# Performance work log

Hardware: AMD Instinct MI355X
Metric: run time of the kernel (lower is better)

The kernel has to match this reference:

```python
import jax, jax.numpy as jnp
import numpy as np

LATENT_DIM = 512
ASSET_DIM = 8192


def setup_inputs() -> dict:
    key = jax.random.key(0)
    ks = jax.random.split(key, 7)
    d = LATENT_DIM
    s = 1.0 / np.sqrt(d)  # torch Linear default init scale (uniform bound)
    z = jax.random.normal(ks[0], (ASSET_DIM, d), dtype=jnp.float32)
    Wq = jax.random.uniform(ks[1], (d, d), jnp.float32, -s, s)
    Wk = jax.random.uniform(ks[2], (d, d), jnp.float32, -s, s)
    Wv = jax.random.uniform(ks[3], (d, d), jnp.float32, -s, s)
    bq = jax.random.uniform(ks[4], (d,), jnp.float32, -s, s)
    bk = jax.random.uniform(ks[5], (d,), jnp.float32, -s, s)
    bv = jax.random.uniform(ks[6], (d,), jnp.float32, -s, s)
    return {"z": z, "Wq": Wq, "bq": bq, "Wk": Wk, "bk": bk, "Wv": Wv, "bv": bv}


def reference(z, Wq, bq, Wk, bk, Wv, bv):
    # z: (N, D). Single-head self-attention over assets.
    d = z.shape[-1]
    scale = d ** (-0.5)
    q = z @ Wq.T + bq          # (N, D)
    k = z @ Wk.T + bk          # (N, D)
    v = z @ Wv.T + bv          # (N, D)
    scores = jnp.einsum('nd,md->nm', q, k) * scale   # (N, N)
    attn = jax.nn.softmax(scores, axis=-1)
    # Original does attn[:, :, None] * v[None] then sum(dim=1); identical math:
    h = attn @ v               # (N, D)
    return h
```

## Files before the change

### kernel.cpp

```cpp
#include <hip/hip_runtime.h>
#include <hip/hip_bf16.h>
#include <stdint.h>

#define D 512
#define N 8192

typedef __attribute__((ext_vector_type(8))) short short8;
typedef __attribute__((ext_vector_type(4))) float f32x4;

static __device__ __forceinline__ unsigned short f2bf(float f) {
  unsigned int u = __builtin_bit_cast(unsigned int, f);
  u += 0x7fffu + ((u >> 16) & 1u);
  return (unsigned short)(u >> 16);
}
static __device__ __forceinline__ float bf2f(unsigned short s) {
  unsigned int u = ((unsigned int)s) << 16;
  return __builtin_bit_cast(float, u);
}

typedef const __attribute__((address_space(1))) unsigned int* gas_ptr;
typedef __attribute__((address_space(3))) unsigned int* las_ptr;
static __device__ __forceinline__ void gload_lds16(const void* g, void* l) {
  __builtin_amdgcn_global_load_lds((gas_ptr)g, (las_ptr)l, 16, 0, 0);
}

__global__ void cast_z_k(const float* __restrict__ z, unsigned short* __restrict__ zb) {
  int i = blockIdx.x * 256 + threadIdx.x;
  const int n4 = N * D / 4;
  for (; i < n4; i += gridDim.x * 256) {
    float4 v = ((const float4*)z)[i];
    ushort4 o = { f2bf(v.x), f2bf(v.y), f2bf(v.z), f2bf(v.w) };
    ((ushort4*)zb)[i] = o;
  }
}

__global__ void cast_w_k(const float* __restrict__ Wq, const float* __restrict__ Wk,
                         const float* __restrict__ Wv, const float* __restrict__ bq,
                         const float* __restrict__ bk, const float* __restrict__ bv,
                         unsigned short* __restrict__ wb, float* __restrict__ bqkv) {
  const float scale = 0.044194173824159216f;
  int i = blockIdx.x * 256 + threadIdx.x;
  const int per = D * D / 4;
  if (i < 3 * per) {
    int sec = i / per;
    int w4 = i - sec * per;
    const float* W = sec == 0 ? Wq : (sec == 1 ? Wk : Wv);
    float s = sec == 0 ? scale : 1.0f;
    float4 v = ((const float4*)W)[w4];
    ushort4 o = { f2bf(v.x * s), f2bf(v.y * s), f2bf(v.z * s), f2bf(v.w * s) };
    ((ushort4*)wb)[sec * per + w4] = o;
  }
  if (i < 3 * D) {
    int sec = i >> 9, j = i & (D - 1);
    const float* b = sec == 0 ? bq : (sec == 1 ? bk : bv);
    bqkv[i] = b[j] * (sec == 0 ? scale : 1.0f);
  }
}

#define BM 128
#define BN 128
#define BK 64

template <int EPI>
__global__ __launch_bounds__(256) void gemm_nt(
    const unsigned short* __restrict__ A, int lda,
    const unsigned short* __restrict__ B, int ldb,
    int K, int tiles_n,
    const float* __restrict__ bias,
    unsigned short* __restrict__ o0, unsigned short* __restrict__ o1,
    unsigned short* __restrict__ o2,
    float* __restrict__ lpart) {
  __shared__ unsigned short Ash[2][BM * BK];
  __shared__ unsigned short Bsh[2][BN * BK];

  const int t = threadIdx.x;
  const int w = t >> 6, lane = t & 63;
  const int bid = blockIdx.x, nwg = gridDim.x;
  const int cpx = nwg >> 3;
  const int swz = (bid & 7) * cpx + (bid >> 3);
  int tm, tn, kt0 = 0, nkt = K / BK, sidx = 0;
  if constexpr (EPI == 3) {
    sidx = swz >> 8;
    const int tile = swz & 255;
    tm = tile >> 2;
    tn = tile & 3;
    kt0 = sidx * 43;
    nkt = (sidx < 2) ? 43 : 42;
  } else {
    tm = swz / tiles_n;
    tn = swz - tm * tiles_n;
  }
  const int row0 = tm * BM, col0 = tn * BN;

  const int srow = t >> 3;
  const int scol = ((t & 7) ^ ((t >> 3) & 7)) * 8;
  const unsigned short* Ab = A + (size_t)(row0 + srow) * lda + scol;
  const unsigned short* Bb = B + (size_t)(col0 + srow) * ldb + scol;
  const int ldsbase = (w * 64) * 8;

  const int l15 = lane & 15, lhi = lane >> 4, lx = lane & 7;
  const int wr = w >> 1, wc = w & 1;
  const int arow = (wr * 64 + l15) * BK;
  const int brow = (wc * 64 + l15) * BK;
  const int ko0 = ((0 + lhi) ^ lx) * 8;
  const int ko1 = ((4 + lhi) ^ lx) * 8;

  f32x4 acc[4][4] = {};

  auto stage = [&](int buf, int k0) {
    const unsigned short* a = Ab + k0;
    const unsigned short* b = Bb + k0;
    unsigned short* la = &Ash[buf][ldsbase];
    unsigned short* lb = &Bsh[buf][ldsbase];
#pragma unroll
    for (int i = 0; i < 4; ++i) {
      gload_lds16(a + (size_t)(i * 32) * lda, la + i * 2048);
      gload_lds16(b + (size_t)(i * 32) * ldb, lb + i * 2048);
    }
  };

  stage(0, kt0 * BK);
  asm volatile("s_waitcnt vmcnt(0)" ::: "memory");
  __syncthreads();
  int cur = 0;
  for (int kt = 0; kt < nkt; ++kt) {
    if (kt + 1 < nkt) stage(cur ^ 1, (kt0 + kt + 1) * BK);
    const unsigned short* As = Ash[cur];
    const unsigned short* Bs = Bsh[cur];
#pragma unroll
    for (int ks = 0; ks < 2; ++ks) {
      const int ko = ks ? ko1 : ko0;
      short8 af[4], bg[4];
#pragma unroll
      for (int rf = 0; rf < 4; ++rf)
        af[rf] = *(const short8*)(As + arow + rf * (16 * BK) + ko);
#pragma unroll
      for (int cf = 0; cf < 4; ++cf)
        bg[cf] = *(const short8*)(Bs + brow + cf * (16 * BK) + ko);
#pragma unroll
      for (int rf = 0; rf < 4; ++rf)
#pragma unroll
        for (int cf = 0; cf < 4; ++cf)
          acc[rf][cf] = __builtin_amdgcn_mfma_f32_16x16x32_bf16(af[rf], bg[cf], acc[rf][cf], 0, 0, 0);
    }
    asm volatile("s_waitcnt vmcnt(0)" ::: "memory");
    __syncthreads();
    cur ^= 1;
  }

  const int r0g = row0 + wr * 64;
  const int c0g = col0 + wc * 64;

  if constexpr (EPI == 0) {
    const int sec = col0 >> 9;
#pragma unroll
    for (int cf = 0; cf < 4; ++cf) {
      const int c = c0g + cf * 16 + l15;
      const int cj = c & (D - 1);
      const float bb = bias[c];
#pragma unroll
      for (int rf = 0; rf < 4; ++rf) {
        const int r = r0g + rf * 16 + lhi * 4;
        f32x4 v = acc[rf][cf];
        if (sec == 0) {
#pragma unroll
          for (int g = 0; g < 4; ++g) o0[(size_t)(r + g) * D + cj] = f2bf(v[g] + bb);
        } else if (sec == 1) {
#pragma unroll
          for (int g = 0; g < 4; ++g) o1[(size_t)(r + g) * D + cj] = f2bf(v[g] + bb);
        } else {
          ushort4 o = { f2bf(v[0] + bb), f2bf(v[1] + bb), f2bf(v[2] + bb), f2bf(v[3] + bb) };
          *(ushort4*)(o2 + (size_t)cj * N + r) = o;
        }
      }
    }
  }

  if constexpr (EPI == 1) {
    float rs[4][4];
#pragma unroll
    for (int rf = 0; rf < 4; ++rf)
#pragma unroll
      for (int g = 0; g < 4; ++g) rs[rf][g] = 0.f;
#pragma unroll
    for (int cf = 0; cf < 4; ++cf) {
      const int c = c0g + cf * 16 + l15;
#pragma unroll
      for (int rf = 0; rf < 4; ++rf) {
        const int r = r0g + rf * 16 + lhi * 4;
        f32x4 v = acc[rf][cf];
#pragma unroll
        for (int g = 0; g < 4; ++g) {
          unsigned short us = f2bf(__expf(v[g]));
          o0[(size_t)(r + g) * N + c] = us;
          rs[rf][g] += bf2f(us);
        }
      }
    }
#pragma unroll
    for (int rf = 0; rf < 4; ++rf)
#pragma unroll
      for (int g = 0; g < 4; ++g) {
        float s = rs[rf][g];
        s += __shfl_xor(s, 1);
        s += __shfl_xor(s, 2);
        s += __shfl_xor(s, 4);
        s += __shfl_xor(s, 8);
        rs[rf][g] = s;
      }
    if (l15 == 0) {
      const int slot = tn * 2 + wc;
#pragma unroll
      for (int rf = 0; rf < 4; ++rf)
#pragma unroll
        for (int g = 0; g < 4; ++g)
          lpart[(size_t)slot * N + r0g + rf * 16 + lhi * 4 + g] = rs[rf][g];
    }
  }

  if constexpr (EPI == 3) {
    unsigned short* op = o0 + (size_t)sidx * ((size_t)N * D);
#pragma unroll
    for (int cf = 0; cf < 4; ++cf) {
      const int c = c0g + cf * 16 + l15;
#pragma unroll
      for (int rf = 0; rf < 4; ++rf) {
        const int r = r0g + rf * 16 + lhi * 4;
        f32x4 v = acc[rf][cf];
#pragma unroll
        for (int g = 0; g < 4; ++g) op[(size_t)(r + g) * D + c] = f2bf(v[g]);
      }
    }
  }
}

__global__ void linv_k(const float* __restrict__ lpart, float* __restrict__ linv) {
  const int m = blockIdx.x * 256 + threadIdx.x;
  float s = 0.f;
  for (int i = 0; i < 128; ++i) s += lpart[(size_t)i * N + m];
  linv[m] = 1.0f / s;
}

__global__ void reduce_k(const unsigned short* __restrict__ Opart,
                         const float* __restrict__ linv, float* __restrict__ out) {
  const int i = blockIdx.x * 256 + threadIdx.x;
  const int m = i >> 7;
  const float li = linv[m];
  const size_t nd = (size_t)N * D;
  ushort4 a = ((const ushort4*)Opart)[i];
  ushort4 b = ((const ushort4*)(Opart + nd))[i];
  ushort4 c = ((const ushort4*)(Opart + 2 * nd))[i];
  float4 o;
  o.x = (bf2f(a.x) + bf2f(b.x) + bf2f(c.x)) * li;
  o.y = (bf2f(a.y) + bf2f(b.y) + bf2f(c.y)) * li;
  o.z = (bf2f(a.z) + bf2f(b.z) + bf2f(c.z)) * li;
  o.w = (bf2f(a.w) + bf2f(b.w) + bf2f(c.w)) * li;
  ((float4*)out)[i] = o;
}

extern "C" void kernel_launch(void* const* d_in, const int* in_sizes, int n_in,
                              void* d_out, int out_size, void* d_ws, size_t ws_size,
                              hipStream_t stream) {
  const float* z  = (const float*)d_in[0];
  const float* Wq = (const float*)d_in[1];
  const float* bq = (const float*)d_in[2];
  const float* Wk = (const float*)d_in[3];
  const float* bk = (const float*)d_in[4];
  const float* Wv = (const float*)d_in[5];
  const float* bv = (const float*)d_in[6];
  float* out = (float*)d_out;

  char* ws = (char*)d_ws;
  unsigned short* zb = (unsigned short*)(ws + 0);
  unsigned short* qb = (unsigned short*)(ws + 8388608);
  unsigned short* kb = (unsigned short*)(ws + 16777216);
  unsigned short* vT = (unsigned short*)(ws + 25165824);
  unsigned short* wb = (unsigned short*)(ws + 33554432);
  float* linv       = (float*)(ws + 33554432);
  float* bqkv       = (float*)(ws + 35127296);
  float* lpart      = (float*)(ws + 35133440);
  unsigned short* P = (unsigned short*)(ws + 39327744);
  unsigned short* Opart = (unsigned short*)(ws + 0);

  cast_z_k<<<dim3(2048), dim3(256), 0, stream>>>(z, zb);
  cast_w_k<<<dim3(768), dim3(256), 0, stream>>>(Wq, Wk, Wv, bq, bk, bv, wb, bqkv);

  gemm_nt<0><<<dim3(64 * 12), dim3(256), 0, stream>>>(
      zb, D, wb, D, D, 12, bqkv, qb, kb, vT, (float*)nullptr);

  gemm_nt<1><<<dim3(64 * 64), dim3(256), 0, stream>>>(
      qb, D, kb, D, D, 64, (const float*)nullptr, P, (unsigned short*)nullptr,
      (unsigned short*)nullptr, lpart);

  linv_k<<<dim3(32), dim3(256), 0, stream>>>(lpart, linv);

  gemm_nt<3><<<dim3(768), dim3(256), 0, stream>>>(
      P, N, vT, N, N, 4, (const float*)nullptr, Opart, (unsigned short*)nullptr,
      (unsigned short*)nullptr, (float*)nullptr);

  reduce_k<<<dim3(4096), dim3(256), 0, stream>>>(Opart, linv, out);
}
```

Before: 269.4 us.

## Replace QK^T exp GEMM with 256x256-tile 8-phase pipelined kernel

Adds a dedicated QK^T kernel that computes exp(scores), writes P and the per-row partial sums. It uses 256x256 output tiles, 512 threads and a double-buffered LDS schedule split into eight phases, with fine-grained barriers and raised MFMA priority. It replaces the generic 128x128 gemm_nt<1> path. The aim is more operand reuse per tile and overlap of global-to-LDS loads with MFMA work. In exchange it uses a large LDS footprint (about 128KB), which limits occupancy, and a more fragile hand-scheduled synchronisation pattern.

```diff
diff --git a/kernel.cpp b/kernel.cpp
--- a/kernel.cpp
+++ b/kernel.cpp
@@ -68,8 +68,7 @@
     int K, int tiles_n,
     const float* __restrict__ bias,
     unsigned short* __restrict__ o0, unsigned short* __restrict__ o1,
-    unsigned short* __restrict__ o2,
-    float* __restrict__ lpart) {
+    unsigned short* __restrict__ o2) {
   __shared__ unsigned short Ash[2][BM * BK];
   __shared__ unsigned short Bsh[2][BN * BK];
 
@@ -176,12 +175,8 @@
     }
   }
 
-  if constexpr (EPI == 1) {
-    float rs[4][4];
-#pragma unroll
-    for (int rf = 0; rf < 4; ++rf)
-#pragma unroll
-      for (int g = 0; g < 4; ++g) rs[rf][g] = 0.f;
+  if constexpr (EPI == 3) {
+    unsigned short* op = o0 + (size_t)sidx * ((size_t)N * D);
 #pragma unroll
     for (int cf = 0; cf < 4; ++cf) {
       const int c = c0g + cf * 16 + l15;
@@ -190,48 +185,168 @@
         const int r = r0g + rf * 16 + lhi * 4;
         f32x4 v = acc[rf][cf];
 #pragma unroll
-        for (int g = 0; g < 4; ++g) {
-          unsigned short us = f2bf(__expf(v[g]));
-          o0[(size_t)(r + g) * N + c] = us;
-          rs[rf][g] += bf2f(us);
-        }
-      }
-    }
-#pragma unroll
-    for (int rf = 0; rf < 4; ++rf)
-#pragma unroll
-      for (int g = 0; g < 4; ++g) {
-        float s = rs[rf][g];
-        s += __shfl_xor(s, 1);
-        s += __shfl_xor(s, 2);
-        s += __shfl_xor(s, 4);
-        s += __shfl_xor(s, 8);
-        rs[rf][g] = s;
-      }
-    if (l15 == 0) {
-      const int slot = tn * 2 + wc;
-#pragma unroll
-      for (int rf = 0; rf < 4; ++rf)
-#pragma unroll
-        for (int g = 0; g < 4; ++g)
-          lpart[(size_t)slot * N + r0g + rf * 16 + lhi * 4 + g] = rs[rf][g];
-    }
-  }
-
-  if constexpr (EPI == 3) {
-    unsigned short* op = o0 + (size_t)sidx * ((size_t)N * D);
-#pragma unroll
-    for (int cf = 0; cf < 4; ++cf) {
-      const int c = c0g + cf * 16 + l15;
-#pragma unroll
-      for (int rf = 0; rf < 4; ++rf) {
-        const int r = r0g + rf * 16 + lhi * 4;
-        f32x4 v = acc[rf][cf];
-#pragma unroll
         for (int g = 0; g < 4; ++g) op[(size_t)(r + g) * D + c] = f2bf(v[g]);
       }
     }
   }
+}
+
+__global__ __launch_bounds__(512, 2) void qk_exp_8ph(
+    const unsigned short* __restrict__ A,
+    const unsigned short* __restrict__ B,
+    unsigned short* __restrict__ P,
+    float* __restrict__ lpart) {
+  __shared__ unsigned short Ash[2][256 * 64];
+  __shared__ unsigned short Bsh[2][256 * 64];
+
+  const int t = threadIdx.x;
+  const int w = t >> 6, lane = t & 63;
+  const int bid = blockIdx.x;
+  const int swz = (bid & 7) * 128 + (bid >> 3);
+  const int tm = swz >> 5, tn = swz & 31;
+  const int row0 = tm * 256, col0 = tn * 256;
+
+  const int wr = w >> 2, wc = w & 3;
+  const int l15 = lane & 15, lhi = lane >> 4, lx = lane & 7;
+
+  const int sr = t >> 3;
+  const int ss = ((t & 7) ^ (sr & 7)) * 8;
+  const unsigned short* Ab = A + (size_t)(row0 + sr) * D + ss;
+  const unsigned short* Bb = B + (size_t)(col0 + sr) * D + ss;
+  const int ldst = t * 8;
+
+  const int aRowB = (wr * 128 + l15) * 64;
+  const int bRowB = (wc * 64 + l15) * 64;
+  const int sl0 = ((0 + lhi) ^ lx) * 8;
+  const int sl1 = ((4 + lhi) ^ lx) * 8;
+
+  f32x4 acc[8][4] = {};
+  short8 af[4][2], bf[2][2];
+
+#define STAGE8(buf, kt)                                                     \
+  do {                                                                      \
+    const unsigned short* a_ = Ab + (kt) * 64;                              \
+    const unsigned short* b_ = Bb + (kt) * 64;                              \
+    unsigned short* la_ = &Ash[buf][0];                                     \
+    unsigned short* lb_ = &Bsh[buf][0];                                     \
+    gload_lds16(a_, la_ + ldst);                                            \
+    gload_lds16(a_ + (size_t)64 * D, la_ + 4096 + ldst);                    \
+    gload_lds16(a_ + (size_t)128 * D, la_ + 8192 + ldst);                   \
+    gload_lds16(a_ + (size_t)192 * D, la_ + 12288 + ldst);                  \
+    gload_lds16(b_, lb_ + ldst);                                            \
+    gload_lds16(b_ + (size_t)64 * D, lb_ + 4096 + ldst);                    \
+    gload_lds16(b_ + (size_t)128 * D, lb_ + 8192 + ldst);                   \
+    gload_lds16(b_ + (size_t)192 * D, lb_ + 12288 + ldst);                  \
+  } while (0)
+
+#define RDA(kk, mh)                                                          \
+  do {                                                                       \
+    _Pragma("unroll") for (int fm = 0; fm < 4; ++fm) {                       \
+      const unsigned short* p_ = &Ash[kk][aRowB + (mh) * 4096 + fm * 1024];  \
+      af[fm][0] = *(const short8*)(p_ + sl0);                                \
+      af[fm][1] = *(const short8*)(p_ + sl1);                                \
+    }                                                                        \
+  } while (0)
+
+#define RDB(kk, nh)                                                          \
+  do {                                                                       \
+    _Pragma("unroll") for (int fn = 0; fn < 2; ++fn) {                       \
+      const unsigned short* p_ = &Bsh[kk][bRowB + (nh) * 2048 + fn * 1024];  \
+      bf[fn][0] = *(const short8*)(p_ + sl0);                                \
+      bf[fn][1] = *(const short8*)(p_ + sl1);                                \
+    }                                                                        \
+  } while (0)
+
+#define MMA(mh, nh)                                                          \
+  do {                                                                       \
+    __builtin_amdgcn_s_setprio(1);                                           \
+    _Pragma("unroll") for (int ks = 0; ks < 2; ++ks)                         \
+      _Pragma("unroll") for (int fm = 0; fm < 4; ++fm)                       \
+        _Pragma("unroll") for (int fn = 0; fn < 2; ++fn)                     \
+          acc[(mh) * 4 + fm][(nh) * 2 + fn] =                                \
+              __builtin_amdgcn_mfma_f32_16x16x32_bf16(                       \
+                  af[fm][ks], bf[fn][ks], acc[(mh) * 4 + fm][(nh) * 2 + fn], \
+                  0, 0, 0);                                                  \
+    __builtin_amdgcn_s_setprio(0);                                           \
+  } while (0)
+
+#define BARLG()                                         \
+  do {                                                  \
+    __builtin_amdgcn_s_barrier();                       \
+    asm volatile("s_waitcnt lgkmcnt(0)" ::: "memory");  \
+    __builtin_amdgcn_sched_barrier(0);                  \
+  } while (0)
+
+#define VMDRAIN() asm volatile("s_waitcnt vmcnt(0)" ::: "memory")
+#define POSTBAR() __builtin_amdgcn_s_barrier()
+
+  STAGE8(0, 0);
+  VMDRAIN();
+  __builtin_amdgcn_s_barrier();
+
+  const int NI = (D / 64) / 2;
+  for (int i = 0; i < NI; ++i) {
+    RDA(0, 0); RDB(0, 0);
+    STAGE8(1, 2 * i + 1);
+    BARLG(); MMA(0, 0); POSTBAR();
+
+    RDB(0, 1);
+    BARLG(); MMA(0, 1); POSTBAR();
+
+    RDA(0, 1);
+    BARLG(); MMA(1, 1); POSTBAR();
+
+    RDB(0, 0);
+    VMDRAIN();
+    BARLG(); MMA(1, 0); POSTBAR();
+
+    RDA(1, 0); RDB(1, 0);
+    if (i + 1 < NI) STAGE8(0, 2 * i + 2);
+    BARLG(); MMA(0, 0); POSTBAR();
+
+    RDB(1, 1);
+    BARLG(); MMA(0, 1); POSTBAR();
+
+    RDA(1, 1);
+    BARLG(); MMA(1, 1); POSTBAR();
+
+    RDB(1, 0);
+    if (i + 1 < NI) VMDRAIN();
+    BARLG(); MMA(1, 0); POSTBAR();
+  }
+
+#pragma unroll
+  for (int fm = 0; fm < 8; ++fm) {
+    const int r = row0 + wr * 128 + fm * 16 + lhi * 4;
+    float rs[4] = {0.f, 0.f, 0.f, 0.f};
+#pragma unroll
+    for (int fn = 0; fn < 4; ++fn) {
+      const int c = col0 + wc * 64 + fn * 16 + l15;
+      f32x4 v = acc[fm][fn];
+#pragma unroll
+      for (int g = 0; g < 4; ++g) {
+        unsigned short us = f2bf(__expf(v[g]));
+        P[(size_t)(r + g) * N + c] = us;
+        rs[g] += bf2f(us);
+      }
+    }
+#pragma unroll
+    for (int g = 0; g < 4; ++g) {
+      float s = rs[g];
+      s += __shfl_xor(s, 1);
+      s += __shfl_xor(s, 2);
+      s += __shfl_xor(s, 4);
+      s += __shfl_xor(s, 8);
+      if (l15 == 0) lpart[(size_t)(tn * 4 + wc) * N + r + g] = s;
+    }
+  }
+#undef STAGE8
+#undef RDA
+#undef RDB
+#undef MMA
+#undef BARLG
+#undef VMDRAIN
+#undef POSTBAR
 }
 
 __global__ void linv_k(const float* __restrict__ lpart, float* __restrict__ linv) {
@@ -286,17 +401,15 @@
   cast_w_k<<<dim3(768), dim3(256), 0, stream>>>(Wq, Wk, Wv, bq, bk, bv, wb, bqkv);
 
   gemm_nt<0><<<dim3(64 * 12), dim3(256), 0, stream>>>(
-      zb, D, wb, D, D, 12, bqkv, qb, kb, vT, (float*)nullptr);
-
-  gemm_nt<1><<<dim3(64 * 64), dim3(256), 0, stream>>>(
-      qb, D, kb, D, D, 64, (const float*)nullptr, P, (unsigned short*)nullptr,
-      (unsigned short*)nullptr, lpart);
+      zb, D, wb, D, D, 12, bqkv, qb, kb, vT);
+
+  qk_exp_8ph<<<dim3(1024), dim3(512), 0, stream>>>(qb, kb, P, lpart);
 
   linv_k<<<dim3(32), dim3(256), 0, stream>>>(lpart, linv);
 
   gemm_nt<3><<<dim3(768), dim3(256), 0, stream>>>(
       P, N, vT, N, N, 4, (const float*)nullptr, Opart, (unsigned short*)nullptr,
-      (unsigned short*)nullptr, (float*)nullptr);
+      (unsigned short*)nullptr);
 
   reduce_k<<<dim3(4096), dim3(256), 0, stream>>>(Opart, linv, out);
 }
```

Result: faster. 254.1 us (-5.7%).

## Rewrite GEMMs as 512-thread kernels with 4-deep LDS ring pipeline

Applied to the files above, without the earlier changes.

Replaces the 256-thread double-buffered GEMM with a 512-thread (8-wave) kernel that keeps a 4-slot LDS ring with two stages in flight, partial waitcnts, raw s_barrier and setprio around the MFMA block. It also reduces row sums per block in LDS (halving lpart slots), uses nontemporal stores for P and partial outputs, and moves the PV split-K from 3 to 4 splits, with the fourth written directly to fp32 out and folded in by reduce_k. The aim is to overlap global loads with MFMA and cut partial-sum traffic, at the cost of more LDS per block (128KB), which may limit occupancy.

```diff
diff --git a/kernel.cpp b/kernel.cpp
--- a/kernel.cpp
+++ b/kernel.cpp
@@ -57,111 +57,113 @@
   }
 }
 
-#define BM 128
-#define BN 128
-#define BK 64
-
 template <int EPI>
-__global__ __launch_bounds__(256) void gemm_nt(
+__global__ __launch_bounds__(512) void mm128_ring(
     const unsigned short* __restrict__ A, int lda,
     const unsigned short* __restrict__ B, int ldb,
-    int K, int tiles_n,
     const float* __restrict__ bias,
     unsigned short* __restrict__ o0, unsigned short* __restrict__ o1,
     unsigned short* __restrict__ o2,
-    float* __restrict__ lpart) {
-  __shared__ unsigned short Ash[2][BM * BK];
-  __shared__ unsigned short Bsh[2][BN * BK];
+    float* __restrict__ lpart, float* __restrict__ outF) {
+  __shared__ unsigned short Ash[4][128 * 64];
+  __shared__ unsigned short Bsh[4][128 * 64];
 
   const int t = threadIdx.x;
   const int w = t >> 6, lane = t & 63;
-  const int bid = blockIdx.x, nwg = gridDim.x;
-  const int cpx = nwg >> 3;
-  const int swz = (bid & 7) * cpx + (bid >> 3);
-  int tm, tn, kt0 = 0, nkt = K / BK, sidx = 0;
-  if constexpr (EPI == 3) {
-    sidx = swz >> 8;
-    const int tile = swz & 255;
-    tm = tile >> 2;
-    tn = tile & 3;
-    kt0 = sidx * 43;
-    nkt = (sidx < 2) ? 43 : 42;
+  const int wr = w >> 2, wc = w & 3;
+  const int l15 = lane & 15, lhi = lane >> 4, lx = lane & 7;
+  const int bid = blockIdx.x;
+
+  int tm, tn, kt0 = 0, nkt, sp = 0;
+  if constexpr (EPI == 0) {
+    const int swz = (bid & 7) * 96 + (bid >> 3);
+    tm = swz / 12; tn = swz - tm * 12; nkt = 8;
+  } else if constexpr (EPI == 1) {
+    const int swz = (bid & 7) * 512 + (bid >> 3);
+    tm = swz >> 6; tn = swz & 63; nkt = 8;
   } else {
-    tm = swz / tiles_n;
-    tn = swz - tm * tiles_n;
-  }
-  const int row0 = tm * BM, col0 = tn * BN;
-
-  const int srow = t >> 3;
-  const int scol = ((t & 7) ^ ((t >> 3) & 7)) * 8;
-  const unsigned short* Ab = A + (size_t)(row0 + srow) * lda + scol;
-  const unsigned short* Bb = B + (size_t)(col0 + srow) * ldb + scol;
-  const int ldsbase = (w * 64) * 8;
-
-  const int l15 = lane & 15, lhi = lane >> 4, lx = lane & 7;
-  const int wr = w >> 1, wc = w & 1;
-  const int arow = (wr * 64 + l15) * BK;
-  const int brow = (wc * 64 + l15) * BK;
-  const int ko0 = ((0 + lhi) ^ lx) * 8;
-  const int ko1 = ((4 + lhi) ^ lx) * 8;
-
-  f32x4 acc[4][4] = {};
-
-  auto stage = [&](int buf, int k0) {
-    const unsigned short* a = Ab + k0;
-    const unsigned short* b = Bb + k0;
-    unsigned short* la = &Ash[buf][ldsbase];
-    unsigned short* lb = &Bsh[buf][ldsbase];
-#pragma unroll
-    for (int i = 0; i < 4; ++i) {
-      gload_lds16(a + (size_t)(i * 32) * lda, la + i * 2048);
-      gload_lds16(b + (size_t)(i * 32) * ldb, lb + i * 2048);
-    }
+    const int swz = (bid & 7) * 128 + (bid >> 3);
+    sp = swz >> 8;
+    const int idx = swz & 255;
+    tm = idx >> 2; tn = idx & 3;
+    kt0 = sp * 32; nkt = 32;
+  }
+  const int row0 = tm * 128, col0 = tn * 128;
+
+  const int sr = t >> 3;
+  const int sc = ((t & 7) ^ (sr & 7)) * 8;
+  const unsigned short* Ab = A + (size_t)(row0 + sr) * lda + sc;
+  const unsigned short* Bb = B + (size_t)(col0 + sr) * ldb + sc;
+  const int dst = t * 8;
+
+  const int arow = (wr * 64 + l15) * 64;
+  const int brow = (wc * 32 + l15) * 64;
+  const int sl0 = ((0 + lhi) ^ lx) * 8;
+  const int sl1 = ((4 + lhi) ^ lx) * 8;
+
+  f32x4 acc[4][2] = {};
+
+  auto stage = [&](int buf, int kt) {
+    const unsigned short* a = Ab + (size_t)(kt0 + kt) * 64;
+    const unsigned short* b = Bb + (size_t)(kt0 + kt) * 64;
+    gload_lds16(a, &Ash[buf][dst]);
+    gload_lds16(a + (size_t)64 * lda, &Ash[buf][4096 + dst]);
+    gload_lds16(b, &Bsh[buf][dst]);
+    gload_lds16(b + (size_t)64 * ldb, &Bsh[buf][4096 + dst]);
   };
 
-  stage(0, kt0 * BK);
-  asm volatile("s_waitcnt vmcnt(0)" ::: "memory");
-  __syncthreads();
-  int cur = 0;
+  stage(0, 0);
+  stage(1, 1);
+  asm volatile("s_waitcnt vmcnt(4)" ::: "memory");
+  __builtin_amdgcn_s_barrier();
+
   for (int kt = 0; kt < nkt; ++kt) {
-    if (kt + 1 < nkt) stage(cur ^ 1, (kt0 + kt + 1) * BK);
-    const unsigned short* As = Ash[cur];
-    const unsigned short* Bs = Bsh[cur];
-#pragma unroll
-    for (int ks = 0; ks < 2; ++ks) {
-      const int ko = ks ? ko1 : ko0;
-      short8 af[4], bg[4];
-#pragma unroll
-      for (int rf = 0; rf < 4; ++rf)
-        af[rf] = *(const short8*)(As + arow + rf * (16 * BK) + ko);
-#pragma unroll
-      for (int cf = 0; cf < 4; ++cf)
-        bg[cf] = *(const short8*)(Bs + brow + cf * (16 * BK) + ko);
-#pragma unroll
-      for (int rf = 0; rf < 4; ++rf)
-#pragma unroll
-        for (int cf = 0; cf < 4; ++cf)
-          acc[rf][cf] = __builtin_amdgcn_mfma_f32_16x16x32_bf16(af[rf], bg[cf], acc[rf][cf], 0, 0, 0);
-    }
-    asm volatile("s_waitcnt vmcnt(0)" ::: "memory");
-    __syncthreads();
-    cur ^= 1;
-  }
-
-  const int r0g = row0 + wr * 64;
-  const int c0g = col0 + wc * 64;
+    const int kb = kt & 3;
+    short8 af[4][2], bg[2][2];
+#pragma unroll
+    for (int fm = 0; fm < 4; ++fm) {
+      const unsigned short* p = &Ash[kb][arow + fm * 1024];
+      af[fm][0] = *(const short8*)(p + sl0);
+      af[fm][1] = *(const short8*)(p + sl1);
+    }
+#pragma unroll
+    for (int fn = 0; fn < 2; ++fn) {
+      const unsigned short* p = &Bsh[kb][brow + fn * 1024];
+      bg[fn][0] = *(const short8*)(p + sl0);
+      bg[fn][1] = *(const short8*)(p + sl1);
+    }
+    if (kt + 2 < nkt) {
+      stage((kt + 2) & 3, kt + 2);
+      asm volatile("s_waitcnt vmcnt(4)" ::: "memory");
+    } else {
+      asm volatile("s_waitcnt vmcnt(0)" ::: "memory");
+    }
+    __builtin_amdgcn_s_barrier();
+    asm volatile("s_waitcnt lgkmcnt(0)" ::: "memory");
+    __builtin_amdgcn_sched_barrier(0);
+    __builtin_amdgcn_s_setprio(1);
+#pragma unroll
+    for (int ks = 0; ks < 2; ++ks)
+#pragma unroll
+      for (int fm = 0; fm < 4; ++fm)
+#pragma unroll
+        for (int fn = 0; fn < 2; ++fn)
+          acc[fm][fn] = __builtin_amdgcn_mfma_f32_16x16x32_bf16(
+              af[fm][ks], bg[fn][ks], acc[fm][fn], 0, 0, 0);
+    __builtin_amdgcn_s_setprio(0);
+  }
 
   if constexpr (EPI == 0) {
-    const int sec = col0 >> 9;
-#pragma unroll
-    for (int cf = 0; cf < 4; ++cf) {
-      const int c = c0g + cf * 16 + l15;
+    const int sec = tn >> 2;
+#pragma unroll
+    for (int fn = 0; fn < 2; ++fn) {
+      const int c = col0 + wc * 32 + fn * 16 + l15;
       const int cj = c & (D - 1);
       const float bb = bias[c];
 #pragma unroll
-      for (int rf = 0; rf < 4; ++rf) {
-        const int r = r0g + rf * 16 + lhi * 4;
-        f32x4 v = acc[rf][cf];
+      for (int fm = 0; fm < 4; ++fm) {
+        const int r = row0 + wr * 64 + fm * 16 + lhi * 4;
+        f32x4 v = acc[fm][fn];
         if (sec == 0) {
 #pragma unroll
           for (int g = 0; g < 4; ++g) o0[(size_t)(r + g) * D + cj] = f2bf(v[g] + bb);
@@ -179,56 +181,78 @@
   if constexpr (EPI == 1) {
     float rs[4][4];
 #pragma unroll
-    for (int rf = 0; rf < 4; ++rf)
-#pragma unroll
-      for (int g = 0; g < 4; ++g) rs[rf][g] = 0.f;
-#pragma unroll
-    for (int cf = 0; cf < 4; ++cf) {
-      const int c = c0g + cf * 16 + l15;
-#pragma unroll
-      for (int rf = 0; rf < 4; ++rf) {
-        const int r = r0g + rf * 16 + lhi * 4;
-        f32x4 v = acc[rf][cf];
+    for (int fm = 0; fm < 4; ++fm)
+#pragma unroll
+      for (int g = 0; g < 4; ++g) rs[fm][g] = 0.f;
+#pragma unroll
+    for (int fn = 0; fn < 2; ++fn) {
+      const int c = col0 + wc * 32 + fn * 16 + l15;
+#pragma unroll
+      for (int fm = 0; fm < 4; ++fm) {
+        const int r = row0 + wr * 64 + fm * 16 + lhi * 4;
+        f32x4 v = acc[fm][fn];
 #pragma unroll
         for (int g = 0; g < 4; ++g) {
           unsigned short us = f2bf(__expf(v[g]));
-          o0[(size_t)(r + g) * N + c] = us;
-          rs[rf][g] += bf2f(us);
+          __builtin_nontemporal_store(us, &o0[(size_t)(r + g) * N + c]);
+          rs[fm][g] += bf2f(us);
         }
       }
     }
 #pragma unroll
-    for (int rf = 0; rf < 4; ++rf)
+    for (int fm = 0; fm < 4; ++fm)
 #pragma unroll
       for (int g = 0; g < 4; ++g) {
-        float s = rs[rf][g];
+        float s = rs[fm][g];
         s += __shfl_xor(s, 1);
         s += __shfl_xor(s, 2);
         s += __shfl_xor(s, 4);
         s += __shfl_xor(s, 8);
-        rs[rf][g] = s;
-      }
+        rs[fm][g] = s;
+      }
+    __builtin_amdgcn_s_barrier();
+    float* lred = (float*)&Ash[0][0];
     if (l15 == 0) {
-      const int slot = tn * 2 + wc;
-#pragma unroll
-      for (int rf = 0; rf < 4; ++rf)
+#pragma unroll
+      for (int fm = 0; fm < 4; ++fm)
 #pragma unroll
         for (int g = 0; g < 4; ++g)
-          lpart[(size_t)slot * N + r0g + rf * 16 + lhi * 4 + g] = rs[rf][g];
+          lred[wc * 128 + wr * 64 + fm * 16 + lhi * 4 + g] = rs[fm][g];
+    }
+    __syncthreads();
+    if (t < 128) {
+      float s = lred[t] + lred[128 + t] + lred[256 + t] + lred[384 + t];
+      lpart[(size_t)tn * N + row0 + t] = s;
     }
   }
 
   if constexpr (EPI == 3) {
-    unsigned short* op = o0 + (size_t)sidx * ((size_t)N * D);
-#pragma unroll
-    for (int cf = 0; cf < 4; ++cf) {
-      const int c = c0g + cf * 16 + l15;
-#pragma unroll
-      for (int rf = 0; rf < 4; ++rf) {
-        const int r = r0g + rf * 16 + lhi * 4;
-        f32x4 v = acc[rf][cf];
-#pragma unroll
-        for (int g = 0; g < 4; ++g) op[(size_t)(r + g) * D + c] = f2bf(v[g]);
+    if (sp < 3) {
+      unsigned short* op = o0 + (size_t)sp * ((size_t)N * D);
+#pragma unroll
+      for (int fn = 0; fn < 2; ++fn) {
+        const int c = col0 + wc * 32 + fn * 16 + l15;
+#pragma unroll
+        for (int fm = 0; fm < 4; ++fm) {
+          const int r = row0 + wr * 64 + fm * 16 + lhi * 4;
+          f32x4 v = acc[fm][fn];
+#pragma unroll
+          for (int g = 0; g < 4; ++g)
+            __builtin_nontemporal_store(f2bf(v[g]), &op[(size_t)(r + g) * D + c]);
+        }
+      }
+    } else {
+#pragma unroll
+      for (int fn = 0; fn < 2; ++fn) {
+        const int c = col0 + wc * 32 + fn * 16 + l15;
+#pragma unroll
+        for (int fm = 0; fm < 4; ++fm) {
+          const int r = row0 + wr * 64 + fm * 16 + lhi * 4;
+          f32x4 v = acc[fm][fn];
+#pragma unroll
+          for (int g = 0; g < 4; ++g)
+            __builtin_nontemporal_store(v[g], &outF[(size_t)(r + g) * D + c]);
+        }
       }
     }
   }
@@ -237,7 +261,7 @@
 __global__ void linv_k(const float* __restrict__ lpart, float* __restrict__ linv) {
   const int m = blockIdx.x * 256 + threadIdx.x;
   float s = 0.f;
-  for (int i = 0; i < 128; ++i) s += lpart[(size_t)i * N + m];
+  for (int i = 0; i < 64; ++i) s += lpart[(size_t)i * N + m];
   linv[m] = 1.0f / s;
 }
 
@@ -250,11 +274,11 @@
   ushort4 a = ((const ushort4*)Opart)[i];
   ushort4 b = ((const ushort4*)(Opart + nd))[i];
   ushort4 c = ((const ushort4*)(Opart + 2 * nd))[i];
-  float4 o;
-  o.x = (bf2f(a.x) + bf2f(b.x) + bf2f(c.x)) * li;
-  o.y = (bf2f(a.y) + bf2f(b.y) + bf2f(c.y)) * li;
-  o.z = (bf2f(a.z) + bf2f(b.z) + bf2f(c.z)) * li;
-  o.w = (bf2f(a.w) + bf2f(b.w) + bf2f(c.w)) * li;
+  float4 o = ((float4*)out)[i];
+  o.x = (bf2f(a.x) + bf2f(b.x) + bf2f(c.x) + o.x) * li;
+  o.y = (bf2f(a.y) + bf2f(b.y) + bf2f(c.y) + o.y) * li;
+  o.z = (bf2f(a.z) + bf2f(b.z) + bf2f(c.z) + o.z) * li;
+  o.w = (bf2f(a.w) + bf2f(b.w) + bf2f(c.w) + o.w) * li;
   ((float4*)out)[i] = o;
 }
 
@@ -285,18 +309,18 @@
   cast_z_k<<<dim3(2048), dim3(256), 0, stream>>>(z, zb);
   cast_w_k<<<dim3(768), dim3(256), 0, stream>>>(Wq, Wk, Wv, bq, bk, bv, wb, bqkv);
 
-  gemm_nt<0><<<dim3(64 * 12), dim3(256), 0, stream>>>(
-      zb, D, wb, D, D, 12, bqkv, qb, kb, vT, (float*)nullptr);
-
-  gemm_nt<1><<<dim3(64 * 64), dim3(256), 0, stream>>>(
-      qb, D, kb, D, D, 64, (const float*)nullptr, P, (unsigned short*)nullptr,
-      (unsigned short*)nullptr, lpart);
+  mm128_ring<0><<<dim3(768), dim3(512), 0, stream>>>(
+      zb, D, wb, D, bqkv, qb, kb, vT, (float*)nullptr, (float*)nullptr);
+
+  mm128_ring<1><<<dim3(4096), dim3(512), 0, stream>>>(
+      qb, D, kb, D, (const float*)nullptr, P, (unsigned short*)nullptr,
+      (unsigned short*)nullptr, lpart, (float*)nullptr);
 
   linv_k<<<dim3(32), dim3(256), 0, stream>>>(lpart, linv);
 
-  gemm_nt<3><<<dim3(768), dim3(256), 0, stream>>>(
-      P, N, vT, N, N, 4, (const float*)nullptr, Opart, (unsigned short*)nullptr,
-      (unsigned short*)nullptr, (float*)nullptr);
+  mm128_ring<3><<<dim3(1024), dim3(512), 0, stream>>>(
+      P, N, vT, N, (const float*)nullptr, Opart, (unsigned short*)nullptr,
+      (unsigned short*)nullptr, (float*)nullptr, out);
 
   reduce_k<<<dim3(4096), dim3(256), 0, stream>>>(Opart, linv, out);
 }
```

Result: slower. 303.4 us (+12.6%).

## Fuse QK^T, exp and PV into a split-KV attention kernel

Applied to the files above, without the earlier changes.

Replaces the separate scores GEMM (which wrote the full N×N exp matrix to global memory) and the PV GEMM with one fused kernel. Each block handles 128 query rows against a 2048-key split, holding the exp tile in LDS and accumulating P·V in registers. The fourth split writes fp32 straight into the output, and the reduce kernel adds it in. This removes roughly 128MB of P traffic, but uses no running max, only 256 blocks of 512 threads at one block per CU, and no double-buffering of the V loads.

```diff
diff --git a/kernel.cpp b/kernel.cpp
--- a/kernel.cpp
+++ b/kernel.cpp
@@ -57,51 +57,32 @@
   }
 }
 
-#define BM 128
-#define BN 128
-#define BK 64
-
-template <int EPI>
-__global__ __launch_bounds__(256) void gemm_nt(
-    const unsigned short* __restrict__ A, int lda,
-    const unsigned short* __restrict__ B, int ldb,
-    int K, int tiles_n,
+__global__ __launch_bounds__(256) void proj_qkv(
+    const unsigned short* __restrict__ A,
+    const unsigned short* __restrict__ B,
     const float* __restrict__ bias,
     unsigned short* __restrict__ o0, unsigned short* __restrict__ o1,
-    unsigned short* __restrict__ o2,
-    float* __restrict__ lpart) {
-  __shared__ unsigned short Ash[2][BM * BK];
-  __shared__ unsigned short Bsh[2][BN * BK];
+    unsigned short* __restrict__ o2) {
+  __shared__ unsigned short Ash[2][128 * 64];
+  __shared__ unsigned short Bsh[2][128 * 64];
 
   const int t = threadIdx.x;
   const int w = t >> 6, lane = t & 63;
-  const int bid = blockIdx.x, nwg = gridDim.x;
-  const int cpx = nwg >> 3;
-  const int swz = (bid & 7) * cpx + (bid >> 3);
-  int tm, tn, kt0 = 0, nkt = K / BK, sidx = 0;
-  if constexpr (EPI == 3) {
-    sidx = swz >> 8;
-    const int tile = swz & 255;
-    tm = tile >> 2;
-    tn = tile & 3;
-    kt0 = sidx * 43;
-    nkt = (sidx < 2) ? 43 : 42;
-  } else {
-    tm = swz / tiles_n;
-    tn = swz - tm * tiles_n;
-  }
-  const int row0 = tm * BM, col0 = tn * BN;
+  const int bid = blockIdx.x;
+  const int swz = (bid & 7) * 96 + (bid >> 3);
+  const int tm = swz / 12, tn = swz - tm * 12;
+  const int row0 = tm * 128, col0 = tn * 128;
 
   const int srow = t >> 3;
   const int scol = ((t & 7) ^ ((t >> 3) & 7)) * 8;
-  const unsigned short* Ab = A + (size_t)(row0 + srow) * lda + scol;
-  const unsigned short* Bb = B + (size_t)(col0 + srow) * ldb + scol;
+  const unsigned short* Ab = A + (size_t)(row0 + srow) * D + scol;
+  const unsigned short* Bb = B + (size_t)(col0 + srow) * D + scol;
   const int ldsbase = (w * 64) * 8;
 
   const int l15 = lane & 15, lhi = lane >> 4, lx = lane & 7;
   const int wr = w >> 1, wc = w & 1;
-  const int arow = (wr * 64 + l15) * BK;
-  const int brow = (wc * 64 + l15) * BK;
+  const int arow = (wr * 64 + l15) * 64;
+  const int brow = (wc * 64 + l15) * 64;
   const int ko0 = ((0 + lhi) ^ lx) * 8;
   const int ko1 = ((4 + lhi) ^ lx) * 8;
 
@@ -114,17 +95,17 @@
     unsigned short* lb = &Bsh[buf][ldsbase];
 #pragma unroll
     for (int i = 0; i < 4; ++i) {
-      gload_lds16(a + (size_t)(i * 32) * lda, la + i * 2048);
-      gload_lds16(b + (size_t)(i * 32) * ldb, lb + i * 2048);
+      gload_lds16(a + (size_t)(i * 32) * D, la + i * 2048);
+      gload_lds16(b + (size_t)(i * 32) * D, lb + i * 2048);
     }
   };
 
-  stage(0, kt0 * BK);
+  stage(0, 0);
   asm volatile("s_waitcnt vmcnt(0)" ::: "memory");
   __syncthreads();
   int cur = 0;
-  for (int kt = 0; kt < nkt; ++kt) {
-    if (kt + 1 < nkt) stage(cur ^ 1, (kt0 + kt + 1) * BK);
+  for (int kt = 0; kt < 8; ++kt) {
+    if (kt + 1 < 8) stage(cur ^ 1, (kt + 1) * 64);
     const unsigned short* As = Ash[cur];
     const unsigned short* Bs = Bsh[cur];
 #pragma unroll
@@ -133,10 +114,10 @@
       short8 af[4], bg[4];
 #pragma unroll
       for (int rf = 0; rf < 4; ++rf)
-        af[rf] = *(const short8*)(As + arow + rf * (16 * BK) + ko);
+        af[rf] = *(const short8*)(As + arow + rf * (16 * 64) + ko);
 #pragma unroll
       for (int cf = 0; cf < 4; ++cf)
-        bg[cf] = *(const short8*)(Bs + brow + cf * (16 * BK) + ko);
+        bg[cf] = *(const short8*)(Bs + brow + cf * (16 * 64) + ko);
 #pragma unroll
       for (int rf = 0; rf < 4; ++rf)
 #pragma unroll
@@ -150,94 +131,208 @@
 
   const int r0g = row0 + wr * 64;
   const int c0g = col0 + wc * 64;
-
-  if constexpr (EPI == 0) {
-    const int sec = col0 >> 9;
-#pragma unroll
-    for (int cf = 0; cf < 4; ++cf) {
-      const int c = c0g + cf * 16 + l15;
-      const int cj = c & (D - 1);
-      const float bb = bias[c];
-#pragma unroll
-      for (int rf = 0; rf < 4; ++rf) {
-        const int r = r0g + rf * 16 + lhi * 4;
-        f32x4 v = acc[rf][cf];
-        if (sec == 0) {
-#pragma unroll
-          for (int g = 0; g < 4; ++g) o0[(size_t)(r + g) * D + cj] = f2bf(v[g] + bb);
-        } else if (sec == 1) {
-#pragma unroll
-          for (int g = 0; g < 4; ++g) o1[(size_t)(r + g) * D + cj] = f2bf(v[g] + bb);
-        } else {
-          ushort4 o = { f2bf(v[0] + bb), f2bf(v[1] + bb), f2bf(v[2] + bb), f2bf(v[3] + bb) };
-          *(ushort4*)(o2 + (size_t)cj * N + r) = o;
+  const int sec = col0 >> 9;
+#pragma unroll
+  for (int cf = 0; cf < 4; ++cf) {
+    const int c = c0g + cf * 16 + l15;
+    const int cj = c & (D - 1);
+    const float bb = bias[c];
+#pragma unroll
+    for (int rf = 0; rf < 4; ++rf) {
+      const int r = r0g + rf * 16 + lhi * 4;
+      f32x4 v = acc[rf][cf];
+      if (sec == 0) {
+#pragma unroll
+        for (int g = 0; g < 4; ++g) o0[(size_t)(r + g) * D + cj] = f2bf(v[g] + bb);
+      } else if (sec == 1) {
+#pragma unroll
+        for (int g = 0; g < 4; ++g) o1[(size_t)(r + g) * D + cj] = f2bf(v[g] + bb);
+      } else {
+        ushort4 o = { f2bf(v[0] + bb), f2bf(v[1] + bb), f2bf(v[2] + bb), f2bf(v[3] + bb) };
+        *(ushort4*)(o2 + (size_t)cj * N + r) = o;
+      }
+    }
+  }
+}
+
+__global__ __launch_bounds__(512, 1) void fused_attn(
+    const unsigned short* __restrict__ qb,
+    const unsigned short* __restrict__ kb,
+    const unsigned short* __restrict__ vT,
+    unsigned short* __restrict__ Opart,
+    float* __restrict__ outF,
+    float* __restrict__ lpart) {
+  __shared__ unsigned short SA[2][128 * 32];
+  __shared__ unsigned short SB[2][256 * 32];
+  __shared__ unsigned short PL[128 * 260];
+  __shared__ unsigned short VB[512 * 32];
+
+  const int t = threadIdx.x;
+  const int w = t >> 6, lane = t & 63;
+  const int wr = w >> 2, wc = w & 3;
+  const int l15 = lane & 15, lhi = lane >> 4;
+  const int l3 = l15 & 3;
+
+  const int bid = blockIdx.x;
+  const int xcd = bid & 7, loc = bid >> 3;
+  const int sp = xcd >> 1;
+  const int qt = loc + 32 * (xcd & 1);
+  const int r0 = qt * 128;
+  const int kv0 = sp * 2048;
+
+  const int ssl = (t & 3) ^ ((t >> 2) & 3);
+  const unsigned short* qsrc = qb + (size_t)(r0 + (t >> 2)) * D + ssl * 8;
+  const unsigned short* ksrc = kb + (size_t)(kv0 + (t >> 2)) * D + ssl * 8;
+  const unsigned short* vsrc = vT + (size_t)(t >> 2) * N + kv0 + ssl * 8;
+  const int sdst = t * 8;
+
+  const int aoff = (wr * 64 + l15) * 32 + ((lhi ^ l3) << 3);
+  const int boff = (wc * 64 + l15) * 32 + ((lhi ^ l3) << 3);
+  const int voff = (wc * 128 + l15) * 32 + ((lhi ^ l3) << 3);
+  const int poff = (wr * 64 + l15) * 260 + (lhi << 3);
+
+  f32x4 acc_o[4][8] = {};
+  float rs_acc[4][4] = {{0.f,0.f,0.f,0.f},{0.f,0.f,0.f,0.f},{0.f,0.f,0.f,0.f},{0.f,0.f,0.f,0.f}};
+
+  for (int sub = 0; sub < 8; ++sub) {
+    const int kvb = sub * 256;
+
+    f32x4 acc_s[4][4] = {};
+    {
+      int cur = 0;
+      {
+        gload_lds16(qsrc, &SA[0][sdst]);
+        const unsigned short* kp = ksrc + (size_t)kvb * D;
+        gload_lds16(kp, &SB[0][sdst]);
+        gload_lds16(kp + (size_t)128 * D, &SB[0][4096 + sdst]);
+        asm volatile("s_waitcnt vmcnt(0)" ::: "memory");
+        __syncthreads();
+      }
+      for (int kt = 0; kt < 16; ++kt) {
+        if (kt + 1 < 16) {
+          gload_lds16(qsrc + (kt + 1) * 32, &SA[cur ^ 1][sdst]);
+          const unsigned short* kp = ksrc + (size_t)kvb * D + (kt + 1) * 32;
+          gload_lds16(kp, &SB[cur ^ 1][sdst]);
+          gload_lds16(kp + (size_t)128 * D, &SB[cur ^ 1][4096 + sdst]);
         }
-      }
-    }
-  }
-
-  if constexpr (EPI == 1) {
-    float rs[4][4];
-#pragma unroll
-    for (int rf = 0; rf < 4; ++rf)
-#pragma unroll
-      for (int g = 0; g < 4; ++g) rs[rf][g] = 0.f;
-#pragma unroll
-    for (int cf = 0; cf < 4; ++cf) {
-      const int c = c0g + cf * 16 + l15;
-#pragma unroll
-      for (int rf = 0; rf < 4; ++rf) {
-        const int r = r0g + rf * 16 + lhi * 4;
-        f32x4 v = acc[rf][cf];
+        short8 af[4], bg[4];
+#pragma unroll
+        for (int fm = 0; fm < 4; ++fm) af[fm] = *(const short8*)&SA[cur][aoff + fm * 512];
+#pragma unroll
+        for (int fn = 0; fn < 4; ++fn) bg[fn] = *(const short8*)&SB[cur][boff + fn * 512];
+#pragma unroll
+        for (int fm = 0; fm < 4; ++fm)
+#pragma unroll
+          for (int fn = 0; fn < 4; ++fn)
+            acc_s[fm][fn] = __builtin_amdgcn_mfma_f32_16x16x32_bf16(
+                af[fm], bg[fn], acc_s[fm][fn], 0, 0, 0);
+        asm volatile("s_waitcnt vmcnt(0)" ::: "memory");
+        __syncthreads();
+        cur ^= 1;
+      }
+    }
+
+#pragma unroll
+    for (int fm = 0; fm < 4; ++fm) {
+      float r4[4] = {0.f, 0.f, 0.f, 0.f};
+#pragma unroll
+      for (int fn = 0; fn < 4; ++fn) {
+        const int col = wc * 64 + fn * 16 + l15;
+        f32x4 v = acc_s[fm][fn];
 #pragma unroll
         for (int g = 0; g < 4; ++g) {
+          const int row = wr * 64 + fm * 16 + lhi * 4 + g;
           unsigned short us = f2bf(__expf(v[g]));
-          o0[(size_t)(r + g) * N + c] = us;
-          rs[rf][g] += bf2f(us);
+          PL[row * 260 + col] = us;
+          r4[g] += bf2f(us);
         }
       }
-    }
-#pragma unroll
-    for (int rf = 0; rf < 4; ++rf)
 #pragma unroll
       for (int g = 0; g < 4; ++g) {
-        float s = rs[rf][g];
+        float s = r4[g];
         s += __shfl_xor(s, 1);
         s += __shfl_xor(s, 2);
         s += __shfl_xor(s, 4);
         s += __shfl_xor(s, 8);
-        rs[rf][g] = s;
-      }
-    if (l15 == 0) {
-      const int slot = tn * 2 + wc;
-#pragma unroll
-      for (int rf = 0; rf < 4; ++rf)
-#pragma unroll
-        for (int g = 0; g < 4; ++g)
-          lpart[(size_t)slot * N + r0g + rf * 16 + lhi * 4 + g] = rs[rf][g];
-    }
-  }
-
-  if constexpr (EPI == 3) {
-    unsigned short* op = o0 + (size_t)sidx * ((size_t)N * D);
-#pragma unroll
-    for (int cf = 0; cf < 4; ++cf) {
-      const int c = c0g + cf * 16 + l15;
-#pragma unroll
-      for (int rf = 0; rf < 4; ++rf) {
-        const int r = r0g + rf * 16 + lhi * 4;
-        f32x4 v = acc[rf][cf];
-#pragma unroll
-        for (int g = 0; g < 4; ++g) op[(size_t)(r + g) * D + c] = f2bf(v[g]);
-      }
-    }
+        rs_acc[fm][g] += s;
+      }
+    }
+    __syncthreads();
+
+#pragma unroll 1
+    for (int ks = 0; ks < 8; ++ks) {
+      {
+        const unsigned short* vp = vsrc + kvb + ks * 32;
+#pragma unroll
+        for (int i = 0; i < 4; ++i)
+          gload_lds16(vp + (size_t)(i * 128) * N, &VB[i * 4096 + sdst]);
+      }
+      asm volatile("s_waitcnt vmcnt(0)" ::: "memory");
+      __syncthreads();
+      short8 pa[4], vb[8];
+#pragma unroll
+      for (int fm = 0; fm < 4; ++fm)
+        pa[fm] = *(const short8*)&PL[poff + fm * 4160 + ks * 32];
+#pragma unroll
+      for (int fn = 0; fn < 8; ++fn) vb[fn] = *(const short8*)&VB[voff + fn * 512];
+#pragma unroll
+      for (int fm = 0; fm < 4; ++fm)
+#pragma unroll
+        for (int fn = 0; fn < 8; ++fn)
+          acc_o[fm][fn] = __builtin_amdgcn_mfma_f32_16x16x32_bf16(
+              pa[fm], vb[fn], acc_o[fm][fn], 0, 0, 0);
+      __syncthreads();
+    }
+  }
+
+  float* lred = (float*)&SA[0][0];
+  if (l15 == 0) {
+#pragma unroll
+    for (int fm = 0; fm < 4; ++fm)
+#pragma unroll
+      for (int g = 0; g < 4; ++g)
+        lred[wc * 128 + wr * 64 + fm * 16 + lhi * 4 + g] = rs_acc[fm][g];
+  }
+  __syncthreads();
+  if (t < 128) {
+    float s = lred[t] + lred[128 + t] + lred[256 + t] + lred[384 + t];
+    lpart[(size_t)sp * N + r0 + t] = s;
+  }
+
+  if (sp < 3) {
+    unsigned short* op = Opart + (size_t)sp * ((size_t)N * D);
+#pragma unroll
+    for (int fm = 0; fm < 4; ++fm)
+#pragma unroll
+      for (int fn = 0; fn < 8; ++fn) {
+        const int c = wc * 128 + fn * 16 + l15;
+        f32x4 v = acc_o[fm][fn];
+#pragma unroll
+        for (int g = 0; g < 4; ++g) {
+          const int r = r0 + wr * 64 + fm * 16 + lhi * 4 + g;
+          op[(size_t)r * D + c] = f2bf(v[g]);
+        }
+      }
+  } else {
+#pragma unroll
+    for (int fm = 0; fm < 4; ++fm)
+#pragma unroll
+      for (int fn = 0; fn < 8; ++fn) {
+        const int c = wc * 128 + fn * 16 + l15;
+        f32x4 v = acc_o[fm][fn];
+#pragma unroll
+        for (int g = 0; g < 4; ++g) {
+          const int r = r0 + wr * 64 + fm * 16 + lhi * 4 + g;
+          outF[(size_t)r * D + c] = v[g];
+        }
+      }
   }
 }
 
 __global__ void linv_k(const float* __restrict__ lpart, float* __restrict__ linv) {
   const int m = blockIdx.x * 256 + threadIdx.x;
   float s = 0.f;
-  for (int i = 0; i < 128; ++i) s += lpart[(size_t)i * N + m];
+  for (int i = 0; i < 4; ++i) s += lpart[(size_t)i * N + m];
   linv[m] = 1.0f / s;
 }
 
@@ -250,11 +345,11 @@
   ushort4 a = ((const ushort4*)Opart)[i];
   ushort4 b = ((const ushort4*)(Opart + nd))[i];
   ushort4 c = ((const ushort4*)(Opart + 2 * nd))[i];
-  float4 o;
-  o.x = (bf2f(a.x) + bf2f(b.x) + bf2f(c.x)) * li;
-  o.y = (bf2f(a.y) + bf2f(b.y) + bf2f(c.y)) * li;
-  o.z = (bf2f(a.z) + bf2f(b.z) + bf2f(c.z)) * li;
-  o.w = (bf2f(a.w) + bf2f(b.w) + bf2f(c.w)) * li;
+  float4 o = ((float4*)out)[i];
+  o.x = (bf2f(a.x) + bf2f(b.x) + bf2f(c.x) + o.x) * li;
+  o.y = (bf2f(a.y) + bf2f(b.y) + bf2f(c.y) + o.y) * li;
+  o.z = (bf2f(a.z) + bf2f(b.z) + bf2f(c.z) + o.z) * li;
+  o.w = (bf2f(a.w) + bf2f(b.w) + bf2f(c.w) + o.w) * li;
   ((float4*)out)[i] = o;
 }
 
@@ -279,24 +374,16 @@
   float* linv       = (float*)(ws + 33554432);
   float* bqkv       = (float*)(ws + 35127296);
   float* lpart      = (float*)(ws + 35133440);
-  unsigned short* P = (unsigned short*)(ws + 39327744);
-  unsigned short* Opart = (unsigned short*)(ws + 0);
+  unsigned short* Opart = (unsigned short*)(ws + 39327744);
 
   cast_z_k<<<dim3(2048), dim3(256), 0, stream>>>(z, zb);
   cast_w_k<<<dim3(768), dim3(256), 0, stream>>>(Wq, Wk, Wv, bq, bk, bv, wb, bqkv);
 
-  gemm_nt<0><<<dim3(64 * 12), dim3(256), 0, stream>>>(
-      zb, D, wb, D, D, 12, bqkv, qb, kb, vT, (float*)nullptr);
-
-  gemm_nt<1><<<dim3(64 * 64), dim3(256), 0, stream>>>(
-      qb, D, kb, D, D, 64, (const float*)nullptr, P, (unsigned short*)nullptr,
-      (unsigned short*)nullptr, lpart);
+  proj_qkv<<<dim3(768), dim3(256), 0, stream>>>(zb, wb, bqkv, qb, kb, vT);
+
+  fused_attn<<<dim3(256), dim3(512), 0, stream>>>(qb, kb, vT, Opart, out, lpart);
 
   linv_k<<<dim3(32), dim3(256), 0, stream>>>(lpart, linv);
 
-  gemm_nt<3><<<dim3(768), dim3(256), 0, stream>>>(
-      P, N, vT, N, N, 4, (const float*)nullptr, Opart, (unsigned short*)nullptr,
-      (unsigned short*)nullptr, (float*)nullptr);
-
   reduce_k<<<dim3(4096), dim3(256), 0, stream>>>(Opart, linv, out);
 }
```

After: 293.2 us. 1.09x slower.
